# Performance work log

Hardware: AMD Instinct MI355X
Metric: run time of the kernel (lower is better)

Reference implementation:

```python
import jax, jax.numpy as jnp
import numpy as np

NX, NY = 512, 512  # BEV grid size (init_kwargs nx, ny)


def setup_inputs() -> dict:
    key = jax.random.key(0)
    k_emb, k_coord, k_mask = jax.random.split(key, 3)
    B, P, C = 4, 12000, 64
    pillar_embeddings = jax.random.normal(k_emb, (B, P, C), dtype=jnp.float32)
    # unique grid cells per batch (real voxelization never maps two pillars to one cell)
    flat = jax.vmap(lambda k: jax.random.permutation(k, NX * NY)[:P])(
        jax.random.split(k_coord, B))
    pillar_coords = jnp.stack([flat % NX, flat // NX], axis=-1).astype(jnp.int32)  # (ix, iy)
    pillar_mask = jax.random.randint(k_mask, (B, P), 0, 2).astype(jnp.int32)
    return {"pillar_embeddings": pillar_embeddings,
            "pillar_coords": pillar_coords,
            "pillar_mask": pillar_mask}


def reference(pillar_embeddings, pillar_coords, pillar_mask):
    # pillar_embeddings: [B, P, C]; pillar_coords: [B, P, 2] (ix, iy); pillar_mask: [B, P]
    B, P, C = pillar_embeddings.shape
    flat = pillar_coords[..., 1] * NX + pillar_coords[..., 0]          # iy*nx + ix -> [B, P]
    # route invalid pillars to a dummy slot (index NX*NY) that is sliced off afterwards
    idx = jnp.where(pillar_mask > 0, flat, NX * NY)                    # [B, P]
    bev = jnp.zeros((B, NX * NY + 1, C), dtype=pillar_embeddings.dtype)
    bev = bev.at[jnp.arange(B)[:, None], idx].set(pillar_embeddings)   # vectorized scatter
    bev = bev[:, :NX * NY].reshape(B, NY, NX, C)
    return bev.transpose(0, 3, 1, 2)                                   # [B, C, NY, NX]
```

## Files before the change

### kernel.cpp

```cpp
#include <hip/hip_runtime.h>

#define NXc 512
#define NYc 512
#define Bc  4
#define Pc  12000
#define Cc  64
#define CELLS (NXc * NYc)
#define MAPN  (Bc * CELLS)

typedef float fv4 __attribute__((ext_vector_type(4)));
typedef int   iv4 __attribute__((ext_vector_type(4)));

__global__ void map_init_kernel(iv4* __restrict__ map4) {
    const int i = blockIdx.x * blockDim.x + threadIdx.x;
    iv4 m = {-1, -1, -1, -1};
    map4[i] = m;
}

__global__ void map_scatter_kernel(const int* __restrict__ coords,
                                   const int* __restrict__ mask,
                                   int* __restrict__ map) {
    const int p = blockIdx.x * blockDim.x + threadIdx.x;
    if (p >= Bc * Pc) return;
    if (mask[p] <= 0) return;
    const int ix = coords[2 * p];
    const int iy = coords[2 * p + 1];
    const int b = p / Pc;
    map[b * CELLS + iy * NXc + ix] = p;
}

__global__ void __launch_bounds__(256)
bev_gather_kernel(const float* __restrict__ emb,
                  const iv4* __restrict__ map4,
                  fv4* __restrict__ out4) {
    const int t = blockIdx.x * blockDim.x + threadIdx.x;
    const int x4 = t & (NXc / 4 - 1);
    const int y  = (t >> 7) & (NYc - 1);
    const int b  = t >> 16;
    const iv4 m = map4[t];

    const float* e0 = emb + (size_t)(m.x < 0 ? 0 : m.x) * Cc;
    const float* e1 = emb + (size_t)(m.y < 0 ? 0 : m.y) * Cc;
    const float* e2 = emb + (size_t)(m.z < 0 ? 0 : m.z) * Cc;
    const float* e3 = emb + (size_t)(m.w < 0 ? 0 : m.w) * Cc;

    fv4* op = out4 + (size_t)b * Cc * (CELLS / 4) + y * (NXc / 4) + x4;
    #pragma unroll 8
    for (int c = 0; c < Cc; ++c) {
        fv4 v;
        v.x = (m.x >= 0) ? e0[c] : 0.0f;
        v.y = (m.y >= 0) ? e1[c] : 0.0f;
        v.z = (m.z >= 0) ? e2[c] : 0.0f;
        v.w = (m.w >= 0) ? e3[c] : 0.0f;
        __builtin_nontemporal_store(v, op);
        op += CELLS / 4;
    }
}

extern "C" void kernel_launch(void* const* d_in, const int* in_sizes, int n_in,
                              void* d_out, int out_size, void* d_ws, size_t ws_size,
                              hipStream_t stream) {
    const float* emb  = (const float*)d_in[0];
    const int* coords = (const int*)d_in[1];
    const int* mask   = (const int*)d_in[2];
    float* out        = (float*)d_out;
    int* map          = (int*)d_ws;

    map_init_kernel<<<MAPN / 4 / 256, 256, 0, stream>>>((iv4*)map);
    map_scatter_kernel<<<(Bc * Pc + 255) / 256, 256, 0, stream>>>(coords, mask, map);
    bev_gather_kernel<<<MAPN / 4 / 256, 256, 0, stream>>>(emb, (const iv4*)map,
                                                          (fv4*)out);
}
```

Baseline: 281.9 us.

## Replace map-based gather with zero-fill plus direct pillar scatter

Drops the cell-to-pillar map build and the gather pass. The output is now zero-filled with streaming vector stores, then each valid pillar writes its 64 channels directly to their channel-major locations. This removes the map init and scatter traffic and the uncoalesced gather reads. In exchange, the scattered single-float writes to strided rows touch partial cache lines, and correctness relies on the coordinates being unique.

```diff
diff --git a/kernel.cpp b/kernel.cpp
--- a/kernel.cpp
+++ b/kernel.cpp
@@ -6,55 +6,39 @@
 #define Pc  12000
 #define Cc  64
 #define CELLS (NXc * NYc)
-#define MAPN  (Bc * CELLS)
+#define OUT_FV4 (Bc * Cc * (CELLS / 4))
 
 typedef float fv4 __attribute__((ext_vector_type(4)));
-typedef int   iv4 __attribute__((ext_vector_type(4)));
 
-__global__ void map_init_kernel(iv4* __restrict__ map4) {
-    const int i = blockIdx.x * blockDim.x + threadIdx.x;
-    iv4 m = {-1, -1, -1, -1};
-    map4[i] = m;
-}
-
-__global__ void map_scatter_kernel(const int* __restrict__ coords,
-                                   const int* __restrict__ mask,
-                                   int* __restrict__ map) {
-    const int p = blockIdx.x * blockDim.x + threadIdx.x;
-    if (p >= Bc * Pc) return;
-    if (mask[p] <= 0) return;
-    const int ix = coords[2 * p];
-    const int iy = coords[2 * p + 1];
-    const int b = p / Pc;
-    map[b * CELLS + iy * NXc + ix] = p;
+__global__ void __launch_bounds__(256)
+zero_fill_kernel(fv4* __restrict__ out4) {
+    const fv4 z = {0.0f, 0.0f, 0.0f, 0.0f};
+    size_t i = (size_t)blockIdx.x * blockDim.x + threadIdx.x;
+    const size_t stride = (size_t)gridDim.x * blockDim.x;
+    #pragma unroll 4
+    for (; i < (size_t)OUT_FV4; i += stride)
+        __builtin_nontemporal_store(z, out4 + i);
 }
 
 __global__ void __launch_bounds__(256)
-bev_gather_kernel(const float* __restrict__ emb,
-                  const iv4* __restrict__ map4,
-                  fv4* __restrict__ out4) {
-    const int t = blockIdx.x * blockDim.x + threadIdx.x;
-    const int x4 = t & (NXc / 4 - 1);
-    const int y  = (t >> 7) & (NYc - 1);
-    const int b  = t >> 16;
-    const iv4 m = map4[t];
+pillar_scatter_kernel(const float* __restrict__ emb,
+                      const int* __restrict__ coords,
+                      const int* __restrict__ mask,
+                      float* __restrict__ out) {
+    const int g    = blockIdx.x * 4 + (threadIdx.x >> 6);
+    const int lane = threadIdx.x & 63;
 
-    const float* e0 = emb + (size_t)(m.x < 0 ? 0 : m.x) * Cc;
-    const float* e1 = emb + (size_t)(m.y < 0 ? 0 : m.y) * Cc;
-    const float* e2 = emb + (size_t)(m.z < 0 ? 0 : m.z) * Cc;
-    const float* e3 = emb + (size_t)(m.w < 0 ? 0 : m.w) * Cc;
+    if (mask[g] <= 0) return;
 
-    fv4* op = out4 + (size_t)b * Cc * (CELLS / 4) + y * (NXc / 4) + x4;
-    #pragma unroll 8
-    for (int c = 0; c < Cc; ++c) {
-        fv4 v;
-        v.x = (m.x >= 0) ? e0[c] : 0.0f;
-        v.y = (m.y >= 0) ? e1[c] : 0.0f;
-        v.z = (m.z >= 0) ? e2[c] : 0.0f;
-        v.w = (m.w >= 0) ? e3[c] : 0.0f;
-        __builtin_nontemporal_store(v, op);
-        op += CELLS / 4;
-    }
+    const int ix = coords[2 * g];
+    const int iy = coords[2 * g + 1];
+    const int b  = g / Pc;
+    const int cell = iy * NXc + ix;
+
+    const float v = emb[(size_t)g * Cc + lane];
+
+    __builtin_nontemporal_store(
+        v, out + (size_t)(b * Cc + lane) * CELLS + cell);
 }
 
 extern "C" void kernel_launch(void* const* d_in, const int* in_sizes, int n_in,
@@ -64,10 +48,7 @@
     const int* coords = (const int*)d_in[1];
     const int* mask   = (const int*)d_in[2];
     float* out        = (float*)d_out;
-    int* map          = (int*)d_ws;
 
-    map_init_kernel<<<MAPN / 4 / 256, 256, 0, stream>>>((iv4*)map);
-    map_scatter_kernel<<<(Bc * Pc + 255) / 256, 256, 0, stream>>>(coords, mask, map);
-    bev_gather_kernel<<<MAPN / 4 / 256, 256, 0, stream>>>(emb, (const iv4*)map,
-                                                          (fv4*)out);
+    zero_fill_kernel<<<2048, 256, 0, stream>>>((fv4*)out);
+    pillar_scatter_kernel<<<Bc * Pc / 4, 256, 0, stream>>>(emb, coords, mask, out);
 }
```

After: 354.9 us. +25.9%, slower.

## Gather one cell per thread with vectorized embedding row loads

Applied to the files above, without the earlier changes.

The gather kernel now assigns one BEV cell per thread instead of four, loading the whole 64-float embedding row as sixteen float4 vector loads and emitting scalar nontemporal stores across channel planes. The aim is contiguous, wide reads of embedding rows in place of strided scalar reads. The trade-off is scalar rather than 128-bit output stores and a four-times-larger grid, with higher register use from holding sixteen vectors. The map-initialization kernel is also replaced by a hipMemsetAsync filling the map with 0xFF.

```diff
diff --git a/kernel.cpp b/kernel.cpp
--- a/kernel.cpp
+++ b/kernel.cpp
@@ -9,13 +9,6 @@
 #define MAPN  (Bc * CELLS)
 
 typedef float fv4 __attribute__((ext_vector_type(4)));
-typedef int   iv4 __attribute__((ext_vector_type(4)));
-
-__global__ void map_init_kernel(iv4* __restrict__ map4) {
-    const int i = blockIdx.x * blockDim.x + threadIdx.x;
-    iv4 m = {-1, -1, -1, -1};
-    map4[i] = m;
-}
 
 __global__ void map_scatter_kernel(const int* __restrict__ coords,
                                    const int* __restrict__ mask,
@@ -31,29 +24,29 @@
 
 __global__ void __launch_bounds__(256)
 bev_gather_kernel(const float* __restrict__ emb,
-                  const iv4* __restrict__ map4,
-                  fv4* __restrict__ out4) {
-    const int t = blockIdx.x * blockDim.x + threadIdx.x;
-    const int x4 = t & (NXc / 4 - 1);
-    const int y  = (t >> 7) & (NYc - 1);
-    const int b  = t >> 16;
-    const iv4 m = map4[t];
+                  const int* __restrict__ map,
+                  float* __restrict__ out) {
+    const int t    = blockIdx.x * blockDim.x + threadIdx.x;
+    const int cell = t & (CELLS - 1);
+    const int b    = t >> 18;
+    const int m    = map[t];
 
-    const float* e0 = emb + (size_t)(m.x < 0 ? 0 : m.x) * Cc;
-    const float* e1 = emb + (size_t)(m.y < 0 ? 0 : m.y) * Cc;
-    const float* e2 = emb + (size_t)(m.z < 0 ? 0 : m.z) * Cc;
-    const float* e3 = emb + (size_t)(m.w < 0 ? 0 : m.w) * Cc;
+    fv4 v[16];
+    #pragma unroll
+    for (int i = 0; i < 16; ++i) v[i] = (fv4){0.f, 0.f, 0.f, 0.f};
+    if (m >= 0) {
+        const fv4* e = (const fv4*)(emb + (size_t)m * Cc);
+        #pragma unroll
+        for (int i = 0; i < 16; ++i) v[i] = e[i];
+    }
 
-    fv4* op = out4 + (size_t)b * Cc * (CELLS / 4) + y * (NXc / 4) + x4;
-    #pragma unroll 8
-    for (int c = 0; c < Cc; ++c) {
-        fv4 v;
-        v.x = (m.x >= 0) ? e0[c] : 0.0f;
-        v.y = (m.y >= 0) ? e1[c] : 0.0f;
-        v.z = (m.z >= 0) ? e2[c] : 0.0f;
-        v.w = (m.w >= 0) ? e3[c] : 0.0f;
-        __builtin_nontemporal_store(v, op);
-        op += CELLS / 4;
+    float* op = out + (size_t)b * Cc * CELLS + cell;
+    #pragma unroll
+    for (int i = 0; i < 16; ++i) {
+        __builtin_nontemporal_store(v[i].x, op);  op += CELLS;
+        __builtin_nontemporal_store(v[i].y, op);  op += CELLS;
+        __builtin_nontemporal_store(v[i].z, op);  op += CELLS;
+        __builtin_nontemporal_store(v[i].w, op);  op += CELLS;
     }
 }
 
@@ -66,8 +59,7 @@
     float* out        = (float*)d_out;
     int* map          = (int*)d_ws;
 
-    map_init_kernel<<<MAPN / 4 / 256, 256, 0, stream>>>((iv4*)map);
+    hipMemsetAsync(map, 0xFF, (size_t)MAPN * sizeof(int), stream);
     map_scatter_kernel<<<(Bc * Pc + 255) / 256, 256, 0, stream>>>(coords, mask, map);
-    bev_gather_kernel<<<MAPN / 4 / 256, 256, 0, stream>>>(emb, (const iv4*)map,
-                                                          (fv4*)out);
+    bev_gather_kernel<<<MAPN / 256, 256, 0, stream>>>(emb, map, out);
 }
```

Result: no change. 281.2 us (-0.2%).

## Parallelize gather over channels with one thread per output vector; memset map

Applied to the files above, without the earlier changes.

The gather kernel now launches one thread per output float4 across all batch×channel planes, instead of one thread per 4 cells looping over 64 channels. This exposes 64× more threads for latency hiding. The cost is that each thread re-reads the map entry, so the map is read 64 times (mostly from cache), and embedding reads become strided per channel. The map init kernel is replaced with hipMemsetAsync filling 0xFF, which gives the same -1 sentinel.

```diff
diff --git a/kernel.cpp b/kernel.cpp
--- a/kernel.cpp
+++ b/kernel.cpp
@@ -7,15 +7,10 @@
 #define Cc  64
 #define CELLS (NXc * NYc)
 #define MAPN  (Bc * CELLS)
+#define OUT_FV4 (Bc * Cc * (CELLS / 4))
 
 typedef float fv4 __attribute__((ext_vector_type(4)));
 typedef int   iv4 __attribute__((ext_vector_type(4)));
-
-__global__ void map_init_kernel(iv4* __restrict__ map4) {
-    const int i = blockIdx.x * blockDim.x + threadIdx.x;
-    iv4 m = {-1, -1, -1, -1};
-    map4[i] = m;
-}
 
 __global__ void map_scatter_kernel(const int* __restrict__ coords,
                                    const int* __restrict__ mask,
@@ -33,28 +28,26 @@
 bev_gather_kernel(const float* __restrict__ emb,
                   const iv4* __restrict__ map4,
                   fv4* __restrict__ out4) {
-    const int t = blockIdx.x * blockDim.x + threadIdx.x;
-    const int x4 = t & (NXc / 4 - 1);
-    const int y  = (t >> 7) & (NYc - 1);
-    const int b  = t >> 16;
-    const iv4 m = map4[t];
+    const int t     = blockIdx.x * blockDim.x + threadIdx.x;
+    const int cell4 = t & (CELLS / 4 - 1);
+    const int plane = t >> 16;
+    const int c     = plane & (Cc - 1);
+    const int b     = plane >> 6;
 
-    const float* e0 = emb + (size_t)(m.x < 0 ? 0 : m.x) * Cc;
-    const float* e1 = emb + (size_t)(m.y < 0 ? 0 : m.y) * Cc;
-    const float* e2 = emb + (size_t)(m.z < 0 ? 0 : m.z) * Cc;
-    const float* e3 = emb + (size_t)(m.w < 0 ? 0 : m.w) * Cc;
+    const iv4 m = map4[(size_t)b * (CELLS / 4) + cell4];
 
-    fv4* op = out4 + (size_t)b * Cc * (CELLS / 4) + y * (NXc / 4) + x4;
-    #pragma unroll 8
-    for (int c = 0; c < Cc; ++c) {
-        fv4 v;
-        v.x = (m.x >= 0) ? e0[c] : 0.0f;
-        v.y = (m.y >= 0) ? e1[c] : 0.0f;
-        v.z = (m.z >= 0) ? e2[c] : 0.0f;
-        v.w = (m.w >= 0) ? e3[c] : 0.0f;
-        __builtin_nontemporal_store(v, op);
-        op += CELLS / 4;
-    }
+    const float x0 = emb[(size_t)(m.x < 0 ? 0 : m.x) * Cc + c];
+    const float x1 = emb[(size_t)(m.y < 0 ? 0 : m.y) * Cc + c];
+    const float x2 = emb[(size_t)(m.z < 0 ? 0 : m.z) * Cc + c];
+    const float x3 = emb[(size_t)(m.w < 0 ? 0 : m.w) * Cc + c];
+
+    fv4 v;
+    v.x = (m.x >= 0) ? x0 : 0.0f;
+    v.y = (m.y >= 0) ? x1 : 0.0f;
+    v.z = (m.z >= 0) ? x2 : 0.0f;
+    v.w = (m.w >= 0) ? x3 : 0.0f;
+
+    __builtin_nontemporal_store(v, out4 + t);
 }
 
 extern "C" void kernel_launch(void* const* d_in, const int* in_sizes, int n_in,
@@ -66,8 +59,8 @@
     float* out        = (float*)d_out;
     int* map          = (int*)d_ws;
 
-    map_init_kernel<<<MAPN / 4 / 256, 256, 0, stream>>>((iv4*)map);
+    hipMemsetAsync(map, 0xFF, (size_t)MAPN * sizeof(int), stream);
     map_scatter_kernel<<<(Bc * Pc + 255) / 256, 256, 0, stream>>>(coords, mask, map);
-    bev_gather_kernel<<<MAPN / 4 / 256, 256, 0, stream>>>(emb, (const iv4*)map,
-                                                          (fv4*)out);
+    bev_gather_kernel<<<OUT_FV4 / 256, 256, 0, stream>>>(emb, (const iv4*)map,
+                                                         (fv4*)out);
 }
```

Result: no change. 276.9 us (-1.8%).
